# Kernel optimization log

Measured on AMD Instinct MI355X. Metric: run time of the kernel, lower is better.

The kernel has to match this reference:

```python
import jax, jax.numpy as jnp
import numpy as np

ALPHA = 1.0


def _bce_with_logits(x, y):
    # torch BCEWithLogitsLoss (mean): y*softplus(-x) + (1-y)*softplus(x)
    return jnp.mean(y * jax.nn.softplus(-x) + (1.0 - y) * jax.nn.softplus(x))


def _cross_entropy(logits, labels):
    # torch CrossEntropyLoss (mean) with int class labels
    logp = jax.nn.log_softmax(logits, axis=-1)
    return -jnp.mean(jnp.take_along_axis(logp, labels[:, None], axis=-1))


def setup_inputs() -> dict:
    key = jax.random.key(0)
    ks = jax.random.split(key, 6)
    B, T, C = 2097152, 4, 16
    return {
        "y_pred_binary": jax.random.normal(ks[0], (B,), dtype=jnp.float32),
        "y_pred_type": jax.random.normal(ks[1], (B, T), dtype=jnp.float32),
        "y_pred_source": jax.random.normal(ks[2], (B, C), dtype=jnp.float32),
        "y_true_binary": jnp.round(jax.random.uniform(ks[3], (B,), dtype=jnp.float32)),
        "y_true_type": jnp.round(jax.random.uniform(ks[4], (B, T), dtype=jnp.float32)),
        "y_true_source": jax.random.randint(ks[5], (B,), 0, C, dtype=jnp.int32),
    }


def reference(y_pred_binary, y_pred_type, y_pred_source,
              y_true_binary, y_true_type, y_true_source):
    loss = _bce_with_logits(y_pred_binary, y_true_binary)
    loss = loss + _bce_with_logits(y_pred_type, y_true_type)
    loss = loss + _cross_entropy(y_pred_source, y_true_source)

    # Non-differentiable consistency counts (torch computes these under
    # no_grad / via round+argmax, which carry no gradient).
    pb = jax.lax.stop_gradient(y_pred_binary)
    pt = jax.lax.stop_gradient(y_pred_type)
    ps = jax.lax.stop_gradient(y_pred_source)

    binary_c = jax.nn.sigmoid(pb) >= 0.5                     # [B] bool (round(sigmoid))
    type_c = jnp.any(jax.nn.sigmoid(pt) >= 0.5, axis=1)      # [B] bool
    source_c = jnp.argmax(ps, axis=1) > 0                    # [B] bool

    # XOR: exactly one of the pair active -> inconsistent
    cons_ab = jnp.mean((binary_c ^ type_c).astype(jnp.float32))
    cons_ac = jnp.mean((binary_c ^ source_c).astype(jnp.float32))

    loss = loss + ALPHA * cons_ab + ALPHA * cons_ac
    return loss
```

## Files before the change

### kernel.cpp

```cpp
#include <hip/hip_runtime.h>
#include <math.h>

#define L2E 1.44269504088896340736f
#define LN2 0.69314718055994530942f
#define G_BLOCKS 2048

#if __has_builtin(__builtin_amdgcn_exp2f)
__device__ __forceinline__ float fexp2(float x)  { return __builtin_amdgcn_exp2f(x); }
#else
__device__ __forceinline__ float fexp2(float x)  { return __exp2f(x); }
#endif
#if __has_builtin(__builtin_amdgcn_logf)
__device__ __forceinline__ float flog2(float x)  { return __builtin_amdgcn_logf(x); }
#else
__device__ __forceinline__ float flog2(float x)  { return __log2f(x); }
#endif

__device__ __forceinline__ float row_contrib_full(
    const float* __restrict__ pb, const float4* __restrict__ pt4,
    const float4* __restrict__ ps4, const float* __restrict__ tb,
    const float4* __restrict__ tt4, const int* __restrict__ ts,
    const float* __restrict__ psf, int row)
{
    float  xb = pb[row], yb = tb[row];
    int    lab = ts[row];
    float4 xt = pt4[row], yt = tt4[row];
    size_t b = (size_t)row * 4;
    float4 r0 = ps4[b+0], r1 = ps4[b+1], r2 = ps4[b+2], r3 = ps4[b+3];
    float vlab = psf[(size_t)row * 16 + lab];
    float v[16] = { r0.x,r0.y,r0.z,r0.w, r1.x,r1.y,r1.z,r1.w,
                    r2.x,r2.y,r2.z,r2.w, r3.x,r3.y,r3.z,r3.w };
    float s = 0.0f;
    for (int j = 0; j < 16; ++j) s += fexp2(v[j] * L2E);
    float g = fexp2(xb * L2E);
    float p = (1.0f+fexp2(xt.x*L2E))*(1.0f+fexp2(xt.y*L2E))
            * (1.0f+fexp2(xt.z*L2E))*(1.0f+fexp2(xt.w*L2E));
    float c = LN2 * (flog2(s * (1.0f+g)) + 0.25f * flog2(p));
    float dot = xt.x*yt.x + xt.y*yt.y + xt.z*yt.z + xt.w*yt.w;
    c = c - vlab - yb*xb - 0.25f*dot;
    bool bin_c  = (xb >= 0.0f);
    bool type_c = fmaxf(fmaxf(xt.x,xt.y), fmaxf(xt.z,xt.w)) >= 0.0f;
    float mr = v[1];
    for (int j = 2; j < 16; ++j) mr = fmaxf(mr, v[j]);
    bool src_c = (mr > v[0]);
    c += (bin_c != type_c) ? 1.0f : 0.0f;
    c += (bin_c != src_c)  ? 1.0f : 0.0f;
    return c;
}

__global__ __launch_bounds__(256) void multitask_loss_kernel(
    const float*  __restrict__ pb,
    const float4* __restrict__ pt4,
    const float4* __restrict__ ps4,
    const float*  __restrict__ tb,
    const float4* __restrict__ tt4,
    const int*    __restrict__ ts,
    int iters,
    float*        __restrict__ partials)
{
    const int tid  = threadIdx.x;
    const int lane = tid & 63;
    const int wave = tid >> 6;
    const int qz   = lane & 3;
    const int grp  = lane >> 2;

    float acc = 0.0f;

    for (int it = 0; it < iters; ++it) {
        const size_t R = ((size_t)it * G_BLOCKS + blockIdx.x) * 256
                       + (size_t)wave * 64;
        const int row = (int)R + lane;

        float  xb = pb[row];
        float  yb = tb[row];
        int    lab = ts[row];
        float4 xt = pt4[row];
        float4 yt = tt4[row];

        size_t pbase = R * 4;
        float4 q0 = ps4[pbase +   0 + lane];
        float4 q1 = ps4[pbase +  64 + lane];
        float4 q2 = ps4[pbase + 128 + lane];
        float4 q3 = ps4[pbase + 192 + lane];

        float g  = fexp2(xb * L2E);
        float f0 = fexp2(xt.x*L2E), f1 = fexp2(xt.y*L2E);
        float f2 = fexp2(xt.z*L2E), f3 = fexp2(xt.w*L2E);
        float p  = ((1.0f+f0)*(1.0f+f1)) * ((1.0f+f2)*(1.0f+f3));
        float dot = xt.x*yt.x + xt.y*yt.y + xt.z*yt.z + xt.w*yt.w;
        float c = LN2 * (flog2(1.0f+g) + 0.25f*flog2(p)) - yb*xb - 0.25f*dot;
        bool bin_c  = (xb >= 0.0f);
        bool type_c = fmaxf(fmaxf(xt.x,xt.y), fmaxf(xt.z,xt.w)) >= 0.0f;

        float S_own = 1.0f, V_own = 0.0f;
        #pragma unroll
        for (int j = 0; j < 4; ++j) {
            float4 qj = (j==0) ? q0 : (j==1) ? q1 : (j==2) ? q2 : q3;

            float e = fexp2(qj.x*L2E) + fexp2(qj.y*L2E)
                    + fexp2(qj.z*L2E) + fexp2(qj.w*L2E);

            float m4 = fmaxf(fmaxf(qj.x,qj.y), fmaxf(qj.z,qj.w));
            float m3 = fmaxf(fmaxf(qj.y,qj.z), qj.w);
            float Mloc = (qz == 0) ? m3 : m4;

            int labj = __shfl(lab, 16*j + grp, 64);
            float sA  = (labj & 1) ? qj.y : qj.x;
            float sB  = (labj & 1) ? qj.w : qj.z;
            float sel = (labj & 2) ? sB : sA;
            float vlab = __shfl(sel, (lane & ~3) + (labj >> 2), 64);

            float t = e + __shfl_xor(e, 1, 64);
            float S = t + __shfl_xor(t, 2, 64);
            float u = fmaxf(Mloc, __shfl_xor(Mloc, 1, 64));
            float M = fmaxf(u, __shfl_xor(u, 2, 64));
            float v0 = __shfl(qj.x, lane & ~3, 64);

            float Ssgn = (M > v0) ? -S : S;

            float Sb = __shfl(Ssgn, (lane & 15) * 4, 64);
            float Vb = __shfl(vlab, (lane & 15) * 4, 64);
            if ((lane >> 4) == j) { S_own = Sb; V_own = Vb; }
        }

        bool src_c = (S_own < 0.0f);
        c += LN2 * flog2(fabsf(S_own)) - V_own;
        c += (bin_c != type_c) ? 1.0f : 0.0f;
        c += (bin_c != src_c)  ? 1.0f : 0.0f;
        acc += c;
    }

    #pragma unroll
    for (int off = 32; off > 0; off >>= 1)
        acc += __shfl_down(acc, off, 64);

    __shared__ float wsum[4];
    if (lane == 0) wsum[wave] = acc;
    __syncthreads();
    if (tid == 0)
        partials[blockIdx.x] = wsum[0] + wsum[1] + wsum[2] + wsum[3];
}

__global__ __launch_bounds__(256) void reduce_kernel(
    const float* __restrict__ partials, int nblocks,
    const float*  __restrict__ pb,  const float4* __restrict__ pt4,
    const float4* __restrict__ ps4, const float*  __restrict__ tb,
    const float4* __restrict__ tt4, const int*    __restrict__ ts,
    const float*  __restrict__ psf,
    int n_main, int B, float* __restrict__ out, double invB)
{
    double s = 0.0;
    for (int i = threadIdx.x; i < nblocks; i += 256)
        s += (double)partials[i];
    for (int r = n_main + threadIdx.x; r < B; r += 256)
        s += (double)row_contrib_full(pb, pt4, ps4, tb, tt4, ts, psf, r);

    #pragma unroll
    for (int off = 32; off > 0; off >>= 1)
        s += __shfl_down(s, off, 64);

    __shared__ double wsum[4];
    int lane = threadIdx.x & 63;
    int wave = threadIdx.x >> 6;
    if (lane == 0) wsum[wave] = s;
    __syncthreads();
    if (threadIdx.x == 0)
        out[0] = (float)((wsum[0] + wsum[1] + wsum[2] + wsum[3]) * invB);
}

extern "C" void kernel_launch(void* const* d_in, const int* in_sizes, int n_in,
                              void* d_out, int out_size, void* d_ws, size_t ws_size,
                              hipStream_t stream) {
    const float*  pb  = (const float*)d_in[0];
    const float4* pt4 = (const float4*)d_in[1];
    const float4* ps4 = (const float4*)d_in[2];
    const float*  psf = (const float*)d_in[2];
    const float*  tb  = (const float*)d_in[3];
    const float4* tt4 = (const float4*)d_in[4];
    const int*    ts  = (const int*)d_in[5];
    int B = in_sizes[0];

    float* partials = (float*)d_ws;

    int iters  = B / (G_BLOCKS * 256);
    int n_main = iters * G_BLOCKS * 256;

    multitask_loss_kernel<<<G_BLOCKS, 256, 0, stream>>>(pb, pt4, ps4, tb, tt4,
                                                        ts, iters, partials);
    reduce_kernel<<<1, 256, 0, stream>>>(partials, G_BLOCKS,
                                         pb, pt4, ps4, tb, tt4, ts, psf,
                                         n_main, B, (float*)d_out,
                                         1.0 / (double)B);
}
```

Baseline: 260.5 us.

## Process one full source row per thread instead of cooperative four-lane shuffles

Replaces the quad-lane cooperative softmax, where four lanes share a row's logits and combine sums, maxes and label values via many cross-lane shuffles, with a per-thread row computation that loads the full 16-logit row as four float4 loads. This removes the shuffle and select overhead. The trade-off is that per-instruction memory accesses become 64-byte strided across the wave instead of fully coalesced, and register use per thread rises. The tail path reuses the same row routine.

```diff
diff --git a/kernel.cpp b/kernel.cpp
--- a/kernel.cpp
+++ b/kernel.cpp
@@ -16,33 +16,44 @@
 __device__ __forceinline__ float flog2(float x)  { return __log2f(x); }
 #endif
 
-__device__ __forceinline__ float row_contrib_full(
-    const float* __restrict__ pb, const float4* __restrict__ pt4,
-    const float4* __restrict__ ps4, const float* __restrict__ tb,
-    const float4* __restrict__ tt4, const int* __restrict__ ts,
-    const float* __restrict__ psf, int row)
+__device__ __forceinline__ float row_contrib(
+    float xb, float yb, int lab, float4 xt, float4 yt,
+    float4 r0, float4 r1, float4 r2, float4 r3)
 {
-    float  xb = pb[row], yb = tb[row];
-    int    lab = ts[row];
-    float4 xt = pt4[row], yt = tt4[row];
-    size_t b = (size_t)row * 4;
-    float4 r0 = ps4[b+0], r1 = ps4[b+1], r2 = ps4[b+2], r3 = ps4[b+3];
-    float vlab = psf[(size_t)row * 16 + lab];
-    float v[16] = { r0.x,r0.y,r0.z,r0.w, r1.x,r1.y,r1.z,r1.w,
-                    r2.x,r2.y,r2.z,r2.w, r3.x,r3.y,r3.z,r3.w };
-    float s = 0.0f;
-    for (int j = 0; j < 16; ++j) s += fexp2(v[j] * L2E);
-    float g = fexp2(xb * L2E);
-    float p = (1.0f+fexp2(xt.x*L2E))*(1.0f+fexp2(xt.y*L2E))
-            * (1.0f+fexp2(xt.z*L2E))*(1.0f+fexp2(xt.w*L2E));
-    float c = LN2 * (flog2(s * (1.0f+g)) + 0.25f * flog2(p));
-    float dot = xt.x*yt.x + xt.y*yt.y + xt.z*yt.z + xt.w*yt.w;
-    c = c - vlab - yb*xb - 0.25f*dot;
+    float g  = fexp2(xb * L2E);
+
+    float f0 = fexp2(xt.x * L2E), f1 = fexp2(xt.y * L2E);
+    float f2 = fexp2(xt.z * L2E), f3 = fexp2(xt.w * L2E);
+    float p  = ((1.0f + f0) * (1.0f + f1)) * ((1.0f + f2) * (1.0f + f3));
+    float dot = xt.x * yt.x + xt.y * yt.y + xt.z * yt.z + xt.w * yt.w;
+
+    float e0  = fexp2(r0.x * L2E), e1  = fexp2(r0.y * L2E);
+    float e2  = fexp2(r0.z * L2E), e3  = fexp2(r0.w * L2E);
+    float e4  = fexp2(r1.x * L2E), e5  = fexp2(r1.y * L2E);
+    float e6  = fexp2(r1.z * L2E), e7  = fexp2(r1.w * L2E);
+    float e8  = fexp2(r2.x * L2E), e9  = fexp2(r2.y * L2E);
+    float e10 = fexp2(r2.z * L2E), e11 = fexp2(r2.w * L2E);
+    float e12 = fexp2(r3.x * L2E), e13 = fexp2(r3.y * L2E);
+    float e14 = fexp2(r3.z * L2E), e15 = fexp2(r3.w * L2E);
+    float S = (((e0 + e1) + (e2 + e3)) + ((e4 + e5) + (e6 + e7)))
+            + (((e8 + e9) + (e10 + e11)) + ((e12 + e13) + (e14 + e15)));
+
+    float4 rh = (lab & 8) ? ((lab & 4) ? r3 : r2) : ((lab & 4) ? r1 : r0);
+    float  va = (lab & 2) ? ((lab & 1) ? rh.w : rh.z)
+                          : ((lab & 1) ? rh.y : rh.x);
+
+    float m1 = fmaxf(fmaxf(r0.y, r0.z), r0.w);
+    float m2 = fmaxf(fmaxf(r1.x, r1.y), fmaxf(r1.z, r1.w));
+    float m3 = fmaxf(fmaxf(r2.x, r2.y), fmaxf(r2.z, r2.w));
+    float m4 = fmaxf(fmaxf(r3.x, r3.y), fmaxf(r3.z, r3.w));
+    float M  = fmaxf(fmaxf(m1, m2), fmaxf(m3, m4));
+
     bool bin_c  = (xb >= 0.0f);
-    bool type_c = fmaxf(fmaxf(xt.x,xt.y), fmaxf(xt.z,xt.w)) >= 0.0f;
-    float mr = v[1];
-    for (int j = 2; j < 16; ++j) mr = fmaxf(mr, v[j]);
-    bool src_c = (mr > v[0]);
+    bool type_c = fmaxf(fmaxf(xt.x, xt.y), fmaxf(xt.z, xt.w)) >= 0.0f;
+    bool src_c  = (M > r0.x);
+
+    float c = LN2 * (flog2(1.0f + g) + 0.25f * flog2(p) + flog2(S))
+            - va - yb * xb - 0.25f * dot;
     c += (bin_c != type_c) ? 1.0f : 0.0f;
     c += (bin_c != src_c)  ? 1.0f : 0.0f;
     return c;
@@ -58,76 +69,25 @@
     int iters,
     float*        __restrict__ partials)
 {
-    const int tid  = threadIdx.x;
-    const int lane = tid & 63;
-    const int wave = tid >> 6;
-    const int qz   = lane & 3;
-    const int grp  = lane >> 2;
-
+    const int tid = threadIdx.x;
     float acc = 0.0f;
 
-    for (int it = 0; it < iters; ++it) {
-        const size_t R = ((size_t)it * G_BLOCKS + blockIdx.x) * 256
-                       + (size_t)wave * 64;
-        const int row = (int)R + lane;
+    size_t row = (size_t)blockIdx.x * 256 + tid;
+    const size_t step = (size_t)G_BLOCKS * 256;
 
+    for (int it = 0; it < iters; ++it, row += step) {
+        const float4* pr = ps4 + row * 4;
+        float4 r0 = pr[0];
+        float4 r1 = pr[1];
+        float4 r2 = pr[2];
+        float4 r3 = pr[3];
         float  xb = pb[row];
         float  yb = tb[row];
         int    lab = ts[row];
         float4 xt = pt4[row];
         float4 yt = tt4[row];
 
-        size_t pbase = R * 4;
-        float4 q0 = ps4[pbase +   0 + lane];
-        float4 q1 = ps4[pbase +  64 + lane];
-        float4 q2 = ps4[pbase + 128 + lane];
-        float4 q3 = ps4[pbase + 192 + lane];
-
-        float g  = fexp2(xb * L2E);
-        float f0 = fexp2(xt.x*L2E), f1 = fexp2(xt.y*L2E);
-        float f2 = fexp2(xt.z*L2E), f3 = fexp2(xt.w*L2E);
-        float p  = ((1.0f+f0)*(1.0f+f1)) * ((1.0f+f2)*(1.0f+f3));
-        float dot = xt.x*yt.x + xt.y*yt.y + xt.z*yt.z + xt.w*yt.w;
-        float c = LN2 * (flog2(1.0f+g) + 0.25f*flog2(p)) - yb*xb - 0.25f*dot;
-        bool bin_c  = (xb >= 0.0f);
-        bool type_c = fmaxf(fmaxf(xt.x,xt.y), fmaxf(xt.z,xt.w)) >= 0.0f;
-
-        float S_own = 1.0f, V_own = 0.0f;
-        #pragma unroll
-        for (int j = 0; j < 4; ++j) {
-            float4 qj = (j==0) ? q0 : (j==1) ? q1 : (j==2) ? q2 : q3;
-
-            float e = fexp2(qj.x*L2E) + fexp2(qj.y*L2E)
-                    + fexp2(qj.z*L2E) + fexp2(qj.w*L2E);
-
-            float m4 = fmaxf(fmaxf(qj.x,qj.y), fmaxf(qj.z,qj.w));
-            float m3 = fmaxf(fmaxf(qj.y,qj.z), qj.w);
-            float Mloc = (qz == 0) ? m3 : m4;
-
-            int labj = __shfl(lab, 16*j + grp, 64);
-            float sA  = (labj & 1) ? qj.y : qj.x;
-            float sB  = (labj & 1) ? qj.w : qj.z;
-            float sel = (labj & 2) ? sB : sA;
-            float vlab = __shfl(sel, (lane & ~3) + (labj >> 2), 64);
-
-            float t = e + __shfl_xor(e, 1, 64);
-            float S = t + __shfl_xor(t, 2, 64);
-            float u = fmaxf(Mloc, __shfl_xor(Mloc, 1, 64));
-            float M = fmaxf(u, __shfl_xor(u, 2, 64));
-            float v0 = __shfl(qj.x, lane & ~3, 64);
-
-            float Ssgn = (M > v0) ? -S : S;
-
-            float Sb = __shfl(Ssgn, (lane & 15) * 4, 64);
-            float Vb = __shfl(vlab, (lane & 15) * 4, 64);
-            if ((lane >> 4) == j) { S_own = Sb; V_own = Vb; }
-        }
-
-        bool src_c = (S_own < 0.0f);
-        c += LN2 * flog2(fabsf(S_own)) - V_own;
-        c += (bin_c != type_c) ? 1.0f : 0.0f;
-        c += (bin_c != src_c)  ? 1.0f : 0.0f;
-        acc += c;
+        acc += row_contrib(xb, yb, lab, xt, yt, r0, r1, r2, r3);
     }
 
     #pragma unroll
@@ -135,6 +95,8 @@
         acc += __shfl_down(acc, off, 64);
 
     __shared__ float wsum[4];
+    const int lane = tid & 63;
+    const int wave = tid >> 6;
     if (lane == 0) wsum[wave] = acc;
     __syncthreads();
     if (tid == 0)
@@ -146,14 +108,16 @@
     const float*  __restrict__ pb,  const float4* __restrict__ pt4,
     const float4* __restrict__ ps4, const float*  __restrict__ tb,
     const float4* __restrict__ tt4, const int*    __restrict__ ts,
-    const float*  __restrict__ psf,
     int n_main, int B, float* __restrict__ out, double invB)
 {
     double s = 0.0;
     for (int i = threadIdx.x; i < nblocks; i += 256)
         s += (double)partials[i];
-    for (int r = n_main + threadIdx.x; r < B; r += 256)
-        s += (double)row_contrib_full(pb, pt4, ps4, tb, tt4, ts, psf, r);
+    for (int r = n_main + threadIdx.x; r < B; r += 256) {
+        const float4* pr = ps4 + (size_t)r * 4;
+        s += (double)row_contrib(pb[r], tb[r], ts[r], pt4[r], tt4[r],
+                                 pr[0], pr[1], pr[2], pr[3]);
+    }
 
     #pragma unroll
     for (int off = 32; off > 0; off >>= 1)
@@ -174,7 +138,6 @@
     const float*  pb  = (const float*)d_in[0];
     const float4* pt4 = (const float4*)d_in[1];
     const float4* ps4 = (const float4*)d_in[2];
-    const float*  psf = (const float*)d_in[2];
     const float*  tb  = (const float*)d_in[3];
     const float4* tt4 = (const float4*)d_in[4];
     const int*    ts  = (const int*)d_in[5];
@@ -188,7 +151,7 @@
     multitask_loss_kernel<<<G_BLOCKS, 256, 0, stream>>>(pb, pt4, ps4, tb, tt4,
                                                         ts, iters, partials);
     reduce_kernel<<<1, 256, 0, stream>>>(partials, G_BLOCKS,
-                                         pb, pt4, ps4, tb, tt4, ts, psf,
+                                         pb, pt4, ps4, tb, tt4, ts,
                                          n_main, B, (float*)d_out,
                                          1.0 / (double)B);
 }
```

After: 259.3 us. Within noise of the previous version (-0.5%).
